# Performance work log

Measured on AMD Instinct MI355X. Metric: run time of the kernel, lower is better.

Reference implementation:

```python
import jax, jax.numpy as jnp
from jax import lax
import numpy as np

B, T, I, H = 256, 512, 512, 1024

def setup_inputs() -> dict:
    key = jax.random.key(0)
    ks = jax.random.split(key, 6)
    s_ih = 1.0 / np.sqrt(H)
    return {
        "x": jax.random.normal(ks[0], (B, T, I), dtype=jnp.float32),
        "W_ih": jax.random.uniform(ks[1], (4 * H, I), minval=-s_ih, maxval=s_ih, dtype=jnp.float32),
        "W_hh": jax.random.uniform(ks[2], (4 * H, H), minval=-s_ih, maxval=s_ih, dtype=jnp.float32),
        "b_ih": jax.random.uniform(ks[3], (4 * H,), minval=-s_ih, maxval=s_ih, dtype=jnp.float32),
        "b_hh": jax.random.uniform(ks[4], (4 * H,), minval=-s_ih, maxval=s_ih, dtype=jnp.float32),
        "c0": jax.random.normal(ks[5], (B, H), dtype=jnp.float32),  # torch code inits cell state with randn
    }

def reference(x, W_ih, W_hh, b_ih, b_hh, c0):
    # Faithful to LSTMBody.forward: h0 = zeros, c0 = randn (provided as input),
    # per-step nn.LSTMCell; returns the final CELL state (the torch code's `out`).
    h0 = jnp.zeros((x.shape[0], W_hh.shape[1]), dtype=x.dtype)
    Wi_T = W_ih.T  # [I, 4H]
    Wh_T = W_hh.T  # [H, 4H]
    b = b_ih + b_hh

    def step(carry, xt):
        h, c = carry
        gates = xt @ Wi_T + h @ Wh_T + b  # [B, 4H]
        i, f, g, o = jnp.split(gates, 4, axis=-1)  # PyTorch gate order: i, f, g, o
        c_new = jax.nn.sigmoid(f) * c + jax.nn.sigmoid(i) * jnp.tanh(g)
        h_new = jax.nn.sigmoid(o) * jnp.tanh(c_new)
        return (h_new, c_new), None

    xs = jnp.swapaxes(x, 0, 1)  # [T, B, I] for scan over time
    (h, c), _ = lax.scan(step, (h0, c0), xs)
    return c
```

## Files before the change

kernel.cpp:

```cpp
#include <hip/hip_runtime.h>
#include <stdint.h>

#define Bsz 256
#define Tsz 512
#define Isz 512
#define Hsz 1024

typedef __attribute__((ext_vector_type(8))) short short8;
typedef __attribute__((ext_vector_type(4))) float f32x4;

static constexpr size_t XBF_OFF  = 0;
static constexpr size_t WIBF_OFF = 134217728;
static constexpr size_t HBUF_OFF = 138412032;
static constexpr size_t FLAG_OFF = 139460608;
static constexpr size_t WS_NEED  = 139493376;

__device__ __forceinline__ unsigned short f2bf(float f) {
  union { float f; unsigned u; } v; v.f = f;
  unsigned r = v.u + 0x7fff + ((v.u >> 16) & 1);
  return (unsigned short)(r >> 16);
}

__device__ __forceinline__ void cvt8(const float* __restrict__ s, unsigned short* __restrict__ d) {
  float4 a = *(const float4*)s;
  float4 b = *(const float4*)(s + 4);
  union { unsigned short us[8]; uint4 v; } o;
  o.us[0] = f2bf(a.x); o.us[1] = f2bf(a.y); o.us[2] = f2bf(a.z); o.us[3] = f2bf(a.w);
  o.us[4] = f2bf(b.x); o.us[5] = f2bf(b.y); o.us[6] = f2bf(b.z); o.us[7] = f2bf(b.w);
  *(uint4*)d = o.v;
}

__device__ __forceinline__ short8 ld_h(const unsigned short* p) {
  unsigned long long lo = __hip_atomic_load((unsigned long long*)(void*)p,
                                            __ATOMIC_RELAXED, __HIP_MEMORY_SCOPE_AGENT);
  unsigned long long hi = __hip_atomic_load((unsigned long long*)(void*)(p + 4),
                                            __ATOMIC_RELAXED, __HIP_MEMORY_SCOPE_AGENT);
  union { unsigned long long q[2]; short8 s; } u;
  u.q[0] = lo; u.q[1] = hi;
  return u.s;
}

__global__ __launch_bounds__(256)
void init_kernel(const float* __restrict__ x, const float* __restrict__ Wi,
                 unsigned char* __restrict__ ws)
{
  unsigned short* xbf  = (unsigned short*)(ws + XBF_OFF);
  unsigned short* wibf = (unsigned short*)(ws + WIBF_OFF);
  const int bid = blockIdx.x;
  const int tid = threadIdx.x;

  if (bid < 32768) {
    const int rowid = bid * 4 + (tid >> 6);
    const int t = rowid >> 8;
    const int b = rowid & 255;
    const int i = (tid & 63) * 8;
    const float* src = x + ((size_t)b * Tsz + t) * Isz + i;
    unsigned short* dst = xbf + (size_t)rowid * Isz + i;
    cvt8(src, dst);
  } else if (bid < 32768 + 1024) {
    const size_t base = (size_t)(bid - 32768) * 2048 + (size_t)tid * 8;
    cvt8(Wi + base, wibf + base);
  } else {
    const int z = bid - 33792;
    uint4 zero = make_uint4(0u, 0u, 0u, 0u);
    for (size_t j = (size_t)z * 256 + tid; j < 67584; j += (size_t)260 * 256)
      ((uint4*)(ws + HBUF_OFF))[j] = zero;
  }
}

__global__ __launch_bounds__(256, 1)
void lstm_persistent(const float* __restrict__ Wh,
                     const float* __restrict__ b_ih, const float* __restrict__ b_hh,
                     const float* __restrict__ c0, float* __restrict__ out,
                     unsigned char* __restrict__ ws)
{
  const unsigned short* __restrict__ xbf  = (const unsigned short*)(ws + XBF_OFF);
  const unsigned short* __restrict__ wibf = (const unsigned short*)(ws + WIBF_OFF);
  unsigned short* __restrict__ hbuf = (unsigned short*)(ws + HBUF_OFF);
  unsigned* __restrict__ flags = (unsigned*)(ws + FLAG_OFF);

  __shared__ unsigned short WhT[64][1032];
  __shared__ float bias[64];

  const int tid  = threadIdx.x;
  const int bid  = blockIdx.x;
  const int cg   = bid & 63;
  const int rg   = bid >> 6;
  const int wv   = tid >> 6;
  const int lane = tid & 63;
  const int l16  = lane & 15;
  const int quad = lane >> 4;

  {
    const int n  = tid >> 2;
    const int q  = n >> 4, u = n & 15;
    const int gc = q * 1024 + cg * 16 + u;
    const int k0 = (tid & 3) * 256;
    const float* src = Wh + (size_t)gc * Hsz + k0;
    unsigned short* dst = &WhT[n][k0];
    #pragma unroll 4
    for (int k = 0; k < 256; k += 8) cvt8(src + k, dst + k);
  }
  if (tid < 64) {
    const int q = tid >> 4, u = tid & 15;
    const int gc = q * 1024 + cg * 16 + u;
    bias[tid] = b_ih[gc] + b_hh[gc];
  }
  __syncthreads();

  const int rowbase = rg * 64 + wv * 16;
  const int arow    = rowbase + l16;
  const int hcol    = cg * 16 + l16;

  const float bi_r = bias[l16];
  const float bf_r = bias[16 + l16];
  const float bg_r = bias[32 + l16];
  const float bo_r = bias[48 + l16];

  float creg[4];
  #pragma unroll
  for (int r = 0; r < 4; ++r)
    creg[r] = c0[(size_t)(rowbase + quad * 4 + r) * Hsz + hcol];

  const unsigned short* bp[4];
  #pragma unroll
  for (int q = 0; q < 4; ++q)
    bp[q] = wibf + (size_t)(q * 1024 + cg * 16 + l16) * Isz + quad * 8;

  int p = 0;
  for (int t = 0; t < Tsz; ++t) {
    const unsigned short* xt = xbf  + (size_t)t * Bsz * Isz + (size_t)arow * Isz + quad * 8;
    const unsigned short* hp = hbuf + (size_t)p * Bsz * Hsz + (size_t)arow * Hsz + quad * 8;

    f32x4 acc[4];
    #pragma unroll
    for (int q = 0; q < 4; ++q) acc[q] = (f32x4){0.f, 0.f, 0.f, 0.f};

    #pragma unroll 4
    for (int ks = 0; ks < 16; ++ks) {
      const int kk = ks * 32;
      short8 av = *(const short8*)(xt + kk);
      short8 b0 = *(const short8*)(bp[0] + kk);
      short8 b1 = *(const short8*)(bp[1] + kk);
      short8 b2 = *(const short8*)(bp[2] + kk);
      short8 b3 = *(const short8*)(bp[3] + kk);
      acc[0] = __builtin_amdgcn_mfma_f32_16x16x32_bf16(av, b0, acc[0], 0, 0, 0);
      acc[1] = __builtin_amdgcn_mfma_f32_16x16x32_bf16(av, b1, acc[1], 0, 0, 0);
      acc[2] = __builtin_amdgcn_mfma_f32_16x16x32_bf16(av, b2, acc[2], 0, 0, 0);
      acc[3] = __builtin_amdgcn_mfma_f32_16x16x32_bf16(av, b3, acc[3], 0, 0, 0);
    }

    if (t > 0 && tid < 8) {
      const unsigned tgt = 32u * (unsigned)t;
      unsigned* f = &flags[tid * 1024];
      while (__hip_atomic_load(f, __ATOMIC_RELAXED, __HIP_MEMORY_SCOPE_AGENT) < tgt)
        ;
    }
    __syncthreads();

    short8 hv[8];
    #pragma unroll
    for (int j = 0; j < 8; ++j) hv[j] = ld_h(hp + j * 32);

    #pragma unroll
    for (int ks = 0; ks < 32; ++ks) {
      short8 av = hv[ks & 7];
      if (ks + 8 < 32) hv[ks & 7] = ld_h(hp + (ks + 8) * 32);
      const int kk = ks * 32;
      short8 b0 = *(const short8*)(&WhT[l16     ][kk + quad * 8]);
      short8 b1 = *(const short8*)(&WhT[16 + l16][kk + quad * 8]);
      short8 b2 = *(const short8*)(&WhT[32 + l16][kk + quad * 8]);
      short8 b3 = *(const short8*)(&WhT[48 + l16][kk + quad * 8]);
      acc[0] = __builtin_amdgcn_mfma_f32_16x16x32_bf16(av, b0, acc[0], 0, 0, 0);
      acc[1] = __builtin_amdgcn_mfma_f32_16x16x32_bf16(av, b1, acc[1], 0, 0, 0);
      acc[2] = __builtin_amdgcn_mfma_f32_16x16x32_bf16(av, b2, acc[2], 0, 0, 0);
      acc[3] = __builtin_amdgcn_mfma_f32_16x16x32_bf16(av, b3, acc[3], 0, 0, 0);
    }

    unsigned short* hn = hbuf + (size_t)(p ^ 1) * Bsz * Hsz;
    #pragma unroll
    for (int r = 0; r < 4; ++r) {
      float gi = acc[0][r] + bi_r;
      float gf = acc[1][r] + bf_r;
      float gg = acc[2][r] + bg_r;
      float go = acc[3][r] + bo_r;
      float si = 1.f / (1.f + __expf(-gi));
      float sf = 1.f / (1.f + __expf(-gf));
      float tg = 1.f - 2.f / (__expf(2.f * gg) + 1.f);
      float so = 1.f / (1.f + __expf(-go));
      float cn = sf * creg[r] + si * tg;
      creg[r] = cn;
      float tc = 1.f - 2.f / (__expf(2.f * cn) + 1.f);
      __hip_atomic_store(&hn[(size_t)(rowbase + quad * 4 + r) * Hsz + hcol],
                         f2bf(so * tc), __ATOMIC_RELAXED, __HIP_MEMORY_SCOPE_AGENT);
    }

    __syncthreads();
    __atomic_signal_fence(__ATOMIC_SEQ_CST);
    if (tid == 0)
      __hip_atomic_fetch_add(&flags[(bid & 7) * 1024], 1u,
                             __ATOMIC_RELAXED, __HIP_MEMORY_SCOPE_AGENT);
    p ^= 1;
  }

  #pragma unroll
  for (int r = 0; r < 4; ++r)
    out[(size_t)(rowbase + quad * 4 + r) * Hsz + hcol] = creg[r];
}

extern "C" void kernel_launch(void* const* d_in, const int* in_sizes, int n_in,
                              void* d_out, int out_size, void* d_ws, size_t ws_size,
                              hipStream_t stream) {
  const float* x   = (const float*)d_in[0];
  const float* Wi  = (const float*)d_in[1];
  const float* Wh  = (const float*)d_in[2];
  const float* bih = (const float*)d_in[3];
  const float* bhh = (const float*)d_in[4];
  const float* c0  = (const float*)d_in[5];
  float* out = (float*)d_out;
  unsigned char* ws = (unsigned char*)d_ws;

  if (ws_size < WS_NEED) return;

  init_kernel<<<34052, 256, 0, stream>>>(x, Wi, ws);

  void* args[] = { (void*)&Wh, (void*)&bih, (void*)&bhh,
                   (void*)&c0, (void*)&out, (void*)&ws };
  hipLaunchCooperativeKernel((void*)lstm_persistent, dim3(256), dim3(256),
                             args, 0, stream);
}
```

Measured before the change: 10.96 ms.

## Replace global block barrier with per-wave fine-grained h-chunk readiness flags

Drops the block-wide __syncthreads and the 8 shared counter flags. Each wave now publishes its own per-step flag slot (indexed by row group, wave and column group) and waits only for the producers of the h columns it is about to read. The wait is interleaved into the recurrent MFMA loop, so computation can start on chunks that are already ready while later producers are still finishing. This adds many more flag polls inside the inner loop, and it relies on relaxed atomics plus signal fences for memory ordering, which is a correctness risk.

After: 12.79 ms. +16.7%, slower.

```diff
diff --git a/kernel.cpp b/kernel.cpp
--- a/kernel.cpp
+++ b/kernel.cpp
@@ -38,6 +38,10 @@
   union { unsigned long long q[2]; short8 s; } u;
   u.q[0] = lo; u.q[1] = hi;
   return u.s;
+}
+
+__device__ __forceinline__ unsigned ld_flag(const unsigned* p) {
+  return __hip_atomic_load((unsigned*)p, __ATOMIC_RELAXED, __HIP_MEMORY_SCOPE_AGENT);
 }
 
 __global__ __launch_bounds__(256)
@@ -112,6 +116,10 @@
   const int arow    = rowbase + l16;
   const int hcol    = cg * 16 + l16;
 
+  unsigned* const flag_base = flags + (size_t)rg * 2048 + (size_t)wv * 8;
+  unsigned* const myslot    = flag_base + (size_t)cg * 32;
+  unsigned* const poll16    = flag_base + (size_t)l16 * 32;
+
   const float bi_r = bias[l16];
   const float bf_r = bias[16 + l16];
   const float bg_r = bias[32 + l16];
@@ -131,6 +139,7 @@
   for (int t = 0; t < Tsz; ++t) {
     const unsigned short* xt = xbf  + (size_t)t * Bsz * Isz + (size_t)arow * Isz + quad * 8;
     const unsigned short* hp = hbuf + (size_t)p * Bsz * Hsz + (size_t)arow * Hsz + quad * 8;
+    const unsigned tgt = (unsigned)t;
 
     f32x4 acc[4];
     #pragma unroll
@@ -150,13 +159,11 @@
       acc[3] = __builtin_amdgcn_mfma_f32_16x16x32_bf16(av, b3, acc[3], 0, 0, 0);
     }
 
-    if (t > 0 && tid < 8) {
-      const unsigned tgt = 32u * (unsigned)t;
-      unsigned* f = &flags[tid * 1024];
-      while (__hip_atomic_load(f, __ATOMIC_RELAXED, __HIP_MEMORY_SCOPE_AGENT) < tgt)
-        ;
-    }
-    __syncthreads();
+    if (t > 0) {
+      unsigned v = ld_flag(poll16);
+      while (!__all((int)(v >= tgt))) v = ld_flag(poll16);
+      __atomic_signal_fence(__ATOMIC_SEQ_CST);
+    }
 
     short8 hv[8];
     #pragma unroll
@@ -165,7 +172,6 @@
     #pragma unroll
     for (int ks = 0; ks < 32; ++ks) {
       short8 av = hv[ks & 7];
-      if (ks + 8 < 32) hv[ks & 7] = ld_h(hp + (ks + 8) * 32);
       const int kk = ks * 32;
       short8 b0 = *(const short8*)(&WhT[l16     ][kk + quad * 8]);
       short8 b1 = *(const short8*)(&WhT[16 + l16][kk + quad * 8]);
@@ -175,6 +181,17 @@
       acc[1] = __builtin_amdgcn_mfma_f32_16x16x32_bf16(av, b1, acc[1], 0, 0, 0);
       acc[2] = __builtin_amdgcn_mfma_f32_16x16x32_bf16(av, b2, acc[2], 0, 0, 0);
       acc[3] = __builtin_amdgcn_mfma_f32_16x16x32_bf16(av, b3, acc[3], 0, 0, 0);
+      if (ks < 24) {
+        if (t > 0) {
+          unsigned* pa = flag_base + (size_t)(2 * (ks + 8)) * 32;
+          unsigned* pb = pa + 32;
+          unsigned va = ld_flag(pa);
+          unsigned vb = ld_flag(pb);
+          while (va < tgt || vb < tgt) { va = ld_flag(pa); vb = ld_flag(pb); }
+          __atomic_signal_fence(__ATOMIC_SEQ_CST);
+        }
+        hv[ks & 7] = ld_h(hp + (ks + 8) * 32);
+      }
     }
 
     unsigned short* hn = hbuf + (size_t)(p ^ 1) * Bsz * Hsz;
@@ -195,11 +212,9 @@
                          f2bf(so * tc), __ATOMIC_RELAXED, __HIP_MEMORY_SCOPE_AGENT);
     }
 
-    __syncthreads();
-    __atomic_signal_fence(__ATOMIC_SEQ_CST);
-    if (tid == 0)
-      __hip_atomic_fetch_add(&flags[(bid & 7) * 1024], 1u,
-                             __ATOMIC_RELAXED, __HIP_MEMORY_SCOPE_AGENT);
+    asm volatile("s_waitcnt vmcnt(0)" ::: "memory");
+    if (lane == 0)
+      __hip_atomic_store(myslot, tgt + 1u, __ATOMIC_RELAXED, __HIP_MEMORY_SCOPE_AGENT);
     p ^= 1;
   }
 
```
